# Kernel tuning notes

Hardware: AMD Instinct MI355X
Metric: run time of the kernel (lower is better)

The kernel has to match this reference:

```python
import jax, jax.numpy as jnp
import numpy as np

IN_FEATURES = 4096
RANK = 64
NUM_EXPERTS = 8
ALPHA = 64.0
SPARSITY = 0.8
SCALING = ALPHA / RANK  # alpha / rank


def setup_inputs() -> dict:
    key = jax.random.key(0)
    k1, k2, k3, k4 = jax.random.split(key, 4)
    B, S = 4, 4096
    projected_input = jax.random.normal(k1, (B, S, RANK), dtype=jnp.float32)
    routing_weights = jax.random.uniform(k2, (B, S, NUM_EXPERTS), dtype=jnp.float32)
    # Stacked expert A matrices [K, in_features, rank] (kaiming-like init ~ normal here)
    A = jax.random.normal(k3, (NUM_EXPERTS, IN_FEATURES, RANK), dtype=jnp.float32) * 0.02
    sparse_mask = (jax.random.uniform(k4, (NUM_EXPERTS, IN_FEATURES, RANK)) >= SPARSITY).astype(jnp.float32)
    A = A * sparse_mask  # module masks A at init as well
    return {
        "projected_input": projected_input,
        "routing_weights": routing_weights,
        "A": A,
        "sparse_mask": sparse_mask,
    }


def reference(projected_input, routing_weights, A, sparse_mask):
    # A_sparse[k] = A[k] * mask[k]; per expert: scaling * (p @ A_sparse[k].T)
    # then weighted sum over experts with routing_weights[..., k].
    A_eff = (A * sparse_mask) * SCALING          # [k, d, r]
    # Weight the rank-projected input per expert, then contract:
    # wp[b,s,k,r] = routing_weights[b,s,k] * projected_input[b,s,r]
    wp = jnp.einsum("bsk,bsr->bskr", routing_weights, projected_input)
    out = jnp.einsum("bskr,kdr->bsd", wp, A_eff)  # [b, s, in_features]
    return out
```

## Files before the change

### kernel.cpp

```cpp
#include <hip/hip_runtime.h>

#define IN_FEATURES 4096
#define RANK 64
#define NUM_EXPERTS 8
#define KDIM 512
#define TOKENS 16384
#define SCALING 1.0f

#define BM 128
#define BN 128
#define BK 64

typedef __bf16 bf16x8 __attribute__((ext_vector_type(8)));
typedef float f32x4 __attribute__((ext_vector_type(4)));

__device__ __forceinline__ unsigned short f2bf(float f) {
  union { float f; unsigned int u; } v; v.f = f;
  unsigned int u = v.u;
  u += 0x7fffu + ((u >> 16) & 1u);
  return (unsigned short)(u >> 16);
}

__device__ __forceinline__ void gload_lds16(const unsigned short* g, unsigned short* l) {
  __builtin_amdgcn_global_load_lds(
      (const __attribute__((address_space(1))) void*)g,
      (__attribute__((address_space(3))) void*)l,
      16, 0, 0);
}

__global__ void __launch_bounds__(256) q_pack(const float* __restrict__ p,
                                              const float* __restrict__ w,
                                              unsigned short* __restrict__ q) {
  int t = blockIdx.x;
  int i = threadIdx.x;
  int k = i >> 5;
  int rp = (i & 31) * 2;
  float wk = w[t * NUM_EXPERTS + k];
  float p0 = p[t * RANK + rp];
  float p1 = p[t * RANK + rp + 1];
  ushort2 o;
  o.x = f2bf(wk * p0);
  o.y = f2bf(wk * p1);
  *(ushort2*)&q[t * KDIM + k * RANK + rp] = o;
}

__global__ void __launch_bounds__(256) b_pack(const float* __restrict__ A,
                                              const float* __restrict__ mask,
                                              unsigned short* __restrict__ Bt) {
  int d = blockIdx.x;
  int i = threadIdx.x;
  int k = i >> 5;
  int rp = (i & 31) * 2;
  long src = ((long)k * IN_FEATURES + d) * RANK + rp;
  float a0 = A[src] * mask[src] * SCALING;
  float a1 = A[src + 1] * mask[src + 1] * SCALING;
  ushort2 o;
  o.x = f2bf(a0);
  o.y = f2bf(a1);
  *(ushort2*)&Bt[d * KDIM + k * RANK + rp] = o;
}

__global__ void __launch_bounds__(256, 2) gemm_kernel(
    const unsigned short* __restrict__ q,
    const unsigned short* __restrict__ Bt,
    float* __restrict__ out) {
  __shared__ __align__(16) unsigned short sA[BM * BK];
  __shared__ __align__(16) unsigned short sB[BN * BK];

  const int tid = threadIdx.x;
  const int lane = tid & 63;
  const int wid = tid >> 6;
  const int u = lane & 15;
  const int quad = lane >> 4;
  const int wave_m = (wid >> 1) * 64;
  const int wave_n = (wid & 1) * 64;

  const int m0 = blockIdx.y * BM;
  const int n0 = blockIdx.x * BN;

  f32x4 acc[4][4];
#pragma unroll
  for (int i = 0; i < 4; ++i)
#pragma unroll
    for (int j = 0; j < 4; ++j)
      acc[i][j] = (f32x4){0.f, 0.f, 0.f, 0.f};

  const unsigned short* gA[4];
  const unsigned short* gB[4];
  unsigned short* lA[4];
  unsigned short* lB[4];
#pragma unroll
  for (int j = 0; j < 4; ++j) {
    int c = j * 256 + tid;
    int row = c >> 3;
    int logc = (c & 7) ^ (row & 7);
    gA[j] = q  + (long)(m0 + row) * KDIM + logc * 8;
    gB[j] = Bt + (long)(n0 + row) * KDIM + logc * 8;
    lA[j] = sA + c * 8;
    lB[j] = sB + c * 8;
  }

  for (int kt = 0; kt < KDIM; kt += BK) {
#pragma unroll
    for (int j = 0; j < 4; ++j) {
      gload_lds16(gA[j] + kt, lA[j]);
      gload_lds16(gB[j] + kt, lB[j]);
    }
    __syncthreads();

#pragma unroll
    for (int ki = 0; ki < 2; ++ki) {
      bf16x8 af[4], bfr[4];
      const int physbase = ki * 4;
#pragma unroll
      for (int mi = 0; mi < 4; ++mi) {
        int row = wave_m + mi * 16 + u;
        int phys = (physbase + quad) ^ (u & 7);
        af[mi] = *(const bf16x8*)&sA[row * BK + phys * 8];
      }
#pragma unroll
      for (int ni = 0; ni < 4; ++ni) {
        int row = wave_n + ni * 16 + u;
        int phys = (physbase + quad) ^ (u & 7);
        bfr[ni] = *(const bf16x8*)&sB[row * BK + phys * 8];
      }
#pragma unroll
      for (int mi = 0; mi < 4; ++mi)
#pragma unroll
        for (int ni = 0; ni < 4; ++ni)
          acc[mi][ni] = __builtin_amdgcn_mfma_f32_16x16x32_bf16(
              af[mi], bfr[ni], acc[mi][ni], 0, 0, 0);
    }
    __syncthreads();
  }

#pragma unroll
  for (int mi = 0; mi < 4; ++mi) {
#pragma unroll
    for (int r = 0; r < 4; ++r) {
      int row = m0 + wave_m + mi * 16 + quad * 4 + r;
#pragma unroll
      for (int ni = 0; ni < 4; ++ni) {
        int col = n0 + wave_n + ni * 16 + u;
        out[(long)row * IN_FEATURES + col] = acc[mi][ni][r];
      }
    }
  }
}

extern "C" void kernel_launch(void* const* d_in, const int* in_sizes, int n_in,
                              void* d_out, int out_size, void* d_ws, size_t ws_size,
                              hipStream_t stream) {
  const float* p    = (const float*)d_in[0];
  const float* w    = (const float*)d_in[1];
  const float* A    = (const float*)d_in[2];
  const float* mask = (const float*)d_in[3];
  float* out = (float*)d_out;

  unsigned short* q  = (unsigned short*)d_ws;
  unsigned short* Bt = q + (size_t)TOKENS * KDIM;

  q_pack<<<TOKENS, 256, 0, stream>>>(p, w, q);
  b_pack<<<IN_FEATURES, 256, 0, stream>>>(A, mask, Bt);

  dim3 grid(IN_FEATURES / BN, TOKENS / BM);
  gemm_kernel<<<grid, dim3(256), 0, stream>>>(q, Bt, out);
}
```

Baseline: 338.7 us.

## Use 256x256 tiles with 8 waves and a double-buffered ping-pong LDS pipeline

Enlarges the GEMM block tile to 256x256 with 512 threads and double-buffers A and B halves in LDS. Global-to-LDS loads for the next k-tiles are interleaved with MFMA quadrants through fine-grained barriers, s_setprio and explicit vmcnt waits. The aim is to hide global load latency and raise arithmetic intensity per block. The cost is a larger LDS footprint and more accumulator registers, which may lower occupancy, plus more barrier overhead.

```diff
diff --git a/kernel.cpp b/kernel.cpp
--- a/kernel.cpp
+++ b/kernel.cpp
@@ -7,9 +7,11 @@
 #define TOKENS 16384
 #define SCALING 1.0f
 
-#define BM 128
-#define BN 128
+#define BM 256
+#define BN 256
 #define BK 64
+#define NKT (KDIM / BK)
+#define NIT (NKT / 2)
 
 typedef __bf16 bf16x8 __attribute__((ext_vector_type(8)));
 typedef float f32x4 __attribute__((ext_vector_type(4)));
@@ -60,90 +62,153 @@
   *(ushort2*)&Bt[d * KDIM + k * RANK + rp] = o;
 }
 
-__global__ void __launch_bounds__(256, 2) gemm_kernel(
+__global__ void __launch_bounds__(512, 2) gemm_kernel(
     const unsigned short* __restrict__ q,
     const unsigned short* __restrict__ Bt,
     float* __restrict__ out) {
-  __shared__ __align__(16) unsigned short sA[BM * BK];
-  __shared__ __align__(16) unsigned short sB[BN * BK];
+  __shared__ __align__(16) unsigned short sA[2][2][128 * BK];
+  __shared__ __align__(16) unsigned short sB[2][2][128 * BK];
 
   const int tid = threadIdx.x;
   const int lane = tid & 63;
   const int wid = tid >> 6;
   const int u = lane & 15;
   const int quad = lane >> 4;
-  const int wave_m = (wid >> 1) * 64;
-  const int wave_n = (wid & 1) * 64;
+  const int hA = wid >> 2;
+  const int hB = (wid & 3) >> 1;
+  const int rB = (wid & 1) * 64;
+  const int wn = (wid & 3) * 64;
 
   const int m0 = blockIdx.y * BM;
   const int n0 = blockIdx.x * BN;
 
-  f32x4 acc[4][4];
-#pragma unroll
-  for (int i = 0; i < 4; ++i)
+  f32x4 acc[8][4];
+#pragma unroll
+  for (int i = 0; i < 8; ++i)
 #pragma unroll
     for (int j = 0; j < 4; ++j)
       acc[i][j] = (f32x4){0.f, 0.f, 0.f, 0.f};
 
-  const unsigned short* gA[4];
-  const unsigned short* gB[4];
-  unsigned short* lA[4];
-  unsigned short* lB[4];
-#pragma unroll
-  for (int j = 0; j < 4; ++j) {
-    int c = j * 256 + tid;
-    int row = c >> 3;
-    int logc = (c & 7) ^ (row & 7);
-    gA[j] = q  + (long)(m0 + row) * KDIM + logc * 8;
-    gB[j] = Bt + (long)(n0 + row) * KDIM + logc * 8;
-    lA[j] = sA + c * 8;
-    lB[j] = sB + c * 8;
+  const int c0 = tid, c1 = tid + 512;
+  const int row0 = c0 >> 3, row1 = c1 >> 3;
+  const int log0 = (c0 & 7) ^ (row0 & 7), log1 = (c1 & 7) ^ (row1 & 7);
+  const unsigned short* gA0 = q + (m0 + row0) * KDIM + log0 * 8;
+  const unsigned short* gA1 = q + (m0 + row1) * KDIM + log1 * 8;
+  const unsigned short* gB0 = Bt + (n0 + row0) * KDIM + log0 * 8;
+  const unsigned short* gB1 = Bt + (n0 + row1) * KDIM + log1 * 8;
+  const int l0 = c0 * 8, l1 = c1 * 8;
+
+  auto stageA = [&](int buf, int h, int kt) {
+    int ko = (kt & (NKT - 1)) * BK + h * 128 * KDIM;
+    gload_lds16(gA0 + ko, &sA[buf][h][l0]);
+    gload_lds16(gA1 + ko, &sA[buf][h][l1]);
+  };
+  auto stageB = [&](int buf, int h, int kt) {
+    int ko = (kt & (NKT - 1)) * BK + h * 128 * KDIM;
+    gload_lds16(gB0 + ko, &sB[buf][h][l0]);
+    gload_lds16(gB1 + ko, &sB[buf][h][l1]);
+  };
+
+  auto ldA = [&](int buf, int mq, bf16x8 (&a)[2][4]) {
+    const unsigned short* base = sA[buf][hA];
+#pragma unroll
+    for (int ki = 0; ki < 2; ++ki)
+#pragma unroll
+      for (int f = 0; f < 4; ++f) {
+        int r = mq * 64 + f * 16 + u;
+        int phys = (ki * 4 + quad) ^ (r & 7);
+        a[ki][f] = *(const bf16x8*)&base[r * BK + phys * 8];
+      }
+  };
+  auto ldB = [&](int buf, int nq, bf16x8 (&b)[2][2]) {
+    const unsigned short* base = sB[buf][hB];
+#pragma unroll
+    for (int ki = 0; ki < 2; ++ki)
+#pragma unroll
+      for (int g = 0; g < 2; ++g) {
+        int r = rB + nq * 32 + g * 16 + u;
+        int phys = (ki * 4 + quad) ^ (r & 7);
+        b[ki][g] = *(const bf16x8*)&base[r * BK + phys * 8];
+      }
+  };
+  auto mfmaQ = [&](int mq, int nq, bf16x8 (&a)[2][4], bf16x8 (&b)[2][2]) {
+    __builtin_amdgcn_s_setprio(1);
+#pragma unroll
+    for (int ki = 0; ki < 2; ++ki)
+#pragma unroll
+      for (int f = 0; f < 4; ++f)
+#pragma unroll
+        for (int g = 0; g < 2; ++g)
+          acc[mq * 4 + f][nq * 2 + g] = __builtin_amdgcn_mfma_f32_16x16x32_bf16(
+              a[ki][f], b[ki][g], acc[mq * 4 + f][nq * 2 + g], 0, 0, 0);
+    __builtin_amdgcn_s_setprio(0);
+  };
+  auto phase_bar = [&]() {
+    __builtin_amdgcn_sched_barrier(0);
+    __builtin_amdgcn_s_barrier();
+  };
+
+  bf16x8 Ar[2][4], B0r[2][2], B1r[2][2];
+
+  stageB(0, 0, 0); stageB(0, 1, 0);
+  stageA(0, 0, 0); stageA(0, 1, 0);
+  stageB(1, 0, 1); stageB(1, 1, 1);
+  asm volatile("s_waitcnt vmcnt(4)" ::: "memory");
+  phase_bar();
+
+  for (int i = 0; i < NIT; ++i) {
+    const int k1 = 2 * i + 1, k2 = 2 * i + 2, k3 = 2 * i + 3;
+    ldA(0, 0, Ar); ldB(0, 0, B0r);
+    stageA(1, 0, k1);
+    phase_bar();
+    mfmaQ(0, 0, Ar, B0r);
+    phase_bar();
+    ldB(0, 1, B1r);
+    stageA(1, 1, k1);
+    phase_bar();
+    mfmaQ(0, 1, Ar, B1r);
+    phase_bar();
+    ldA(0, 1, Ar);
+    stageB(0, 0, k2);
+    phase_bar();
+    mfmaQ(1, 1, Ar, B1r);
+    phase_bar();
+    stageB(0, 1, k2);
+    phase_bar();
+    mfmaQ(1, 0, Ar, B0r);
+    asm volatile("s_waitcnt vmcnt(4)" ::: "memory");
+    phase_bar();
+    ldA(1, 0, Ar); ldB(1, 0, B0r);
+    stageA(0, 0, k2);
+    phase_bar();
+    mfmaQ(0, 0, Ar, B0r);
+    phase_bar();
+    ldB(1, 1, B1r);
+    stageA(0, 1, k2);
+    phase_bar();
+    mfmaQ(0, 1, Ar, B1r);
+    phase_bar();
+    ldA(1, 1, Ar);
+    stageB(1, 0, k3);
+    phase_bar();
+    mfmaQ(1, 1, Ar, B1r);
+    phase_bar();
+    stageB(1, 1, k3);
+    phase_bar();
+    mfmaQ(1, 0, Ar, B0r);
+    asm volatile("s_waitcnt vmcnt(4)" ::: "memory");
+    phase_bar();
   }
 
-  for (int kt = 0; kt < KDIM; kt += BK) {
-#pragma unroll
-    for (int j = 0; j < 4; ++j) {
-      gload_lds16(gA[j] + kt, lA[j]);
-      gload_lds16(gB[j] + kt, lB[j]);
-    }
-    __syncthreads();
-
-#pragma unroll
-    for (int ki = 0; ki < 2; ++ki) {
-      bf16x8 af[4], bfr[4];
-      const int physbase = ki * 4;
-#pragma unroll
-      for (int mi = 0; mi < 4; ++mi) {
-        int row = wave_m + mi * 16 + u;
-        int phys = (physbase + quad) ^ (u & 7);
-        af[mi] = *(const bf16x8*)&sA[row * BK + phys * 8];
-      }
-#pragma unroll
-      for (int ni = 0; ni < 4; ++ni) {
-        int row = wave_n + ni * 16 + u;
-        int phys = (physbase + quad) ^ (u & 7);
-        bfr[ni] = *(const bf16x8*)&sB[row * BK + phys * 8];
-      }
-#pragma unroll
-      for (int mi = 0; mi < 4; ++mi)
-#pragma unroll
-        for (int ni = 0; ni < 4; ++ni)
-          acc[mi][ni] = __builtin_amdgcn_mfma_f32_16x16x32_bf16(
-              af[mi], bfr[ni], acc[mi][ni], 0, 0, 0);
-    }
-    __syncthreads();
-  }
-
-#pragma unroll
-  for (int mi = 0; mi < 4; ++mi) {
-#pragma unroll
-    for (int r = 0; r < 4; ++r) {
-      int row = m0 + wave_m + mi * 16 + quad * 4 + r;
-#pragma unroll
-      for (int ni = 0; ni < 4; ++ni) {
-        int col = n0 + wave_n + ni * 16 + u;
-        out[(long)row * IN_FEATURES + col] = acc[mi][ni][r];
-      }
+#pragma unroll
+  for (int mf = 0; mf < 8; ++mf) {
+    int row = m0 + hA * 128 + mf * 16 + quad * 4;
+#pragma unroll
+    for (int rr = 0; rr < 4; ++rr) {
+      float* orow = out + (long)(row + rr) * IN_FEATURES + n0 + wn + u;
+#pragma unroll
+      for (int nf = 0; nf < 4; ++nf)
+        orow[nf * 16] = acc[mf][nf][rr];
     }
   }
 }
@@ -164,5 +229,5 @@
   b_pack<<<IN_FEATURES, 256, 0, stream>>>(A, mask, Bt);
 
   dim3 grid(IN_FEATURES / BN, TOKENS / BM);
-  gemm_kernel<<<grid, dim3(256), 0, stream>>>(q, Bt, out);
-}
+  gemm_kernel<<<grid, dim3(512), 0, stream>>>(q, Bt, out);
+}
```

New measurement: 343.7 us. No clear change (+1.5%).
